# Kernel tuning notes

Hardware: AMD Instinct MI355X
Metric: run time of the kernel (lower is better)

Reference implementation:

```python
import jax, jax.numpy as jnp
import numpy as np

DIM = 512  # module's self.dim, used for the softmax scale (note: NOT head dim)

def setup_inputs() -> dict:
    key = jax.random.key(0)
    kq, kk, kv = jax.random.split(key, 3)
    shape = (4, 8, 2048, 64)  # [B, H, S, Dh]
    q = jax.random.normal(kq, shape, dtype=jnp.float32)
    k = jax.random.normal(kk, shape, dtype=jnp.float32)
    v = jax.random.normal(kv, shape, dtype=jnp.float32)
    return {"q": q, "k": k, "v": v, "n": 2048}

def reference(q, k, v, n):
    # scores = q @ k^T, then divide by sqrt(dim) AFTER matmul (as in source)
    scores = jnp.einsum('bhqd,bhkd->bhqk', q, k)
    scale = jnp.sqrt(jnp.asarray(DIM, dtype=scores.dtype))
    p_attn = jax.nn.softmax(scores / scale, axis=-1)
    return jnp.einsum('bhqk,bhkd->bhqd', p_attn, v)
```

## Files before the change

kernel.cpp:

```cpp
#include <hip/hip_runtime.h>


using half8   = __attribute__((ext_vector_type(8))) _Float16;
using half4   = __attribute__((ext_vector_type(4))) _Float16;
using half2v  = __attribute__((ext_vector_type(2))) _Float16;
using f32x4   = __attribute__((ext_vector_type(4))) float;
using f32x16  = __attribute__((ext_vector_type(16))) float;
using int4v   = __attribute__((ext_vector_type(4))) int;
using ushort8 = __attribute__((ext_vector_type(8))) unsigned short;

static __device__ __forceinline__ half2v cvt_pk(float a, float b) {
    return __builtin_bit_cast(half2v, __builtin_amdgcn_cvt_pkrtz(a, b));
}
static __device__ __forceinline__ int cvt_pk_i(float a, float b) {
    return __builtin_bit_cast(int, __builtin_amdgcn_cvt_pkrtz(a, b));
}

#define SEQ   2048
#define DH    64
#define QB    128
#define KVB   64
#define NKVT  (SEQ / KVB)
#define NITER (NKVT / 2)
#define NQB   (SEQ / QB)
#define NBH   32
#define TILE_IMG_BYTES 16384
#define QSCALE (1.4426950408889634f / 22.627416997969522f)

#if __has_builtin(__builtin_amdgcn_exp2f)
#define EXP2F __builtin_amdgcn_exp2f
#else
#define EXP2F exp2f
#endif

#define GLOAD4(dst, ptr) \
    asm volatile("global_load_dwordx4 %0, %1, off" : "=v"(dst) : "v"(ptr) : "memory")

#define WAIT_VM0()                                            \
    do {                                                      \
        asm volatile("s_waitcnt vmcnt(0)" ::: "memory");      \
        __builtin_amdgcn_sched_barrier(0);                    \
    } while (0)

#define LDS_BARRIER()                                         \
    do {                                                      \
        asm volatile("s_waitcnt lgkmcnt(0)" ::: "memory");    \
        __builtin_amdgcn_s_barrier();                         \
    } while (0)

#define LGKM_FENCE()                                          \
    do {                                                      \
        asm volatile("s_waitcnt lgkmcnt(0)" ::: "memory");    \
        __builtin_amdgcn_sched_barrier(0);                    \
    } while (0)

#define PLSWAP(a, b) \
    asm volatile("s_nop 1\n\tv_permlane32_swap_b32 %0, %1" : "+v"(a), "+v"(b))

#define MFMA32(A, B, C) __builtin_amdgcn_mfma_f32_32x32x16_f16((A), (B), (C), 0, 0, 0)

static __device__ __forceinline__ f32x16 z16() {
    f32x16 v;
#pragma unroll
    for (int i = 0; i < 16; ++i) v[i] = 0.f;
    return v;
}

#define SOFTPACK(ST0, ST1, PA)                                            \
    do {                                                                  \
        _Pragma("unroll")                                                 \
        for (int kvs2 = 0; kvs2 < 2; ++kvs2) {                            \
            const f32x16& st_ = kvs2 ? (ST1) : (ST0);                     \
            float p[16];                                                  \
            _Pragma("unroll")                                             \
            for (int r = 0; r < 16; ++r) p[r] = EXP2F(st_[r]);            \
            float s0 = 0.f, s1 = 0.f;                                     \
            _Pragma("unroll")                                             \
            for (int r = 0; r < 8; ++r) { s0 += p[r]; s1 += p[r + 8]; }   \
            lsum += s0 + s1;                                              \
            int m0 = cvt_pk_i(p[0],  p[1]),  m1 = cvt_pk_i(p[2],  p[3]);  \
            int m2 = cvt_pk_i(p[4],  p[5]),  m3 = cvt_pk_i(p[6],  p[7]);  \
            int m4 = cvt_pk_i(p[8],  p[9]),  m5 = cvt_pk_i(p[10], p[11]); \
            int m6 = cvt_pk_i(p[12], p[13]), m7 = cvt_pk_i(p[14], p[15]); \
            PLSWAP(m0, m2); PLSWAP(m1, m3);                               \
            PLSWAP(m4, m6); PLSWAP(m5, m7);                               \
            int4v t0; t0[0] = m0; t0[1] = m1; t0[2] = m2; t0[3] = m3;     \
            int4v t1; t1[0] = m4; t1[1] = m5; t1[2] = m6; t1[3] = m7;     \
            (PA)[2 * kvs2 + 0] = __builtin_bit_cast(half8, t0);           \
            (PA)[2 * kvs2 + 1] = __builtin_bit_cast(half8, t1);           \
        }                                                                 \
    } while (0)

__global__ __launch_bounds__(256)
void prep_kv(const float* __restrict__ Kg, const float* __restrict__ Vg,
             char* __restrict__ ws)
{
    __shared__ unsigned short VT[64][72];
    const int bid = blockIdx.x;
    if (bid < 4096) {
        int id   = bid * 256 + threadIdx.x;
        int col4 = id & 15;
        int row  = (id >> 4) & 63;
        int kvt  = (id >> 10) & 31;
        int bh   = id >> 15;
        f32x4 v = *(const f32x4*)(Kg + ((size_t)(bh * SEQ) + kvt * 64 + row) * DH + col4 * 4);
        half2v lo = cvt_pk(v[0], v[1]);
        half2v hi = cvt_pk(v[2], v[3]);
        half4 h; h[0] = lo[0]; h[1] = lo[1]; h[2] = hi[0]; h[3] = hi[1];
        char* out = ws + (size_t)(bh * 32 + kvt) * TILE_IMG_BYTES
                       + ((row * 128 + col4 * 8) ^ ((row & 7) << 4));
        *(half4*)out = h;
    } else {
        int tb  = bid - 4096;
        int bh  = tb >> 5;
        int kvt = tb & 31;
        int tid = threadIdx.x;

        const float* vg = Vg + (size_t)(bh * SEQ) * DH + (size_t)(kvt * 64) * DH;
#pragma unroll
        for (int rr = 0; rr < 4; ++rr) {
            int kv = rr * 16 + (tid >> 4);
            int d4 = (tid & 15) * 4;
            f32x4 v = *(const f32x4*)(vg + (size_t)kv * DH + d4);
#pragma unroll
            for (int j = 0; j < 4; ++j)
                VT[d4 + j][kv] = __builtin_bit_cast(unsigned short, (_Float16)v[j]);
        }
        __syncthreads();

        int d   = tid >> 2;
        int seg = tid & 3;
        ushort8 h0, h1;
#pragma unroll
        for (int j = 0; j < 16; ++j) {
            int off = seg * 32 + j * 2;
            int kv  = (off ^ ((d & 7) << 4)) >> 1;
            unsigned short val = VT[d][kv];
            if (j < 8) h0[j] = val; else h1[j - 8] = val;
        }
        char* out = ws + (size_t)(bh * 32 + kvt) * TILE_IMG_BYTES + 8192 + d * 128 + seg * 32;
        *(ushort8*)(out)      = h0;
        *(ushort8*)(out + 16) = h1;
    }
}

__global__ __launch_bounds__(256, 2)
void fattn_fwd(const float* __restrict__ Qg, const char* __restrict__ Wimg,
               float* __restrict__ Og)
{
    __shared__ __align__(16) char KVl[4][TILE_IMG_BYTES];

    const int tid  = threadIdx.x;
    const int lane = tid & 63;
    const int wave = tid >> 6;
    const int l31  = lane & 31;
    const int hi   = lane >> 5;

    const int wg  = blockIdx.x;
    const int swz = (wg & 7) * 64 + (wg >> 3);
    const int qb  = swz & (NQB - 1);
    const int bh  = swz >> 4;
    const size_t base = (size_t)bh * (SEQ * DH);

    half8 qfrag[4];
    {
        const int qrow = qb * QB + wave * 32 + l31;
        const float* qp = Qg + base + (size_t)qrow * DH + hi * 8;
#pragma unroll
        for (int ks = 0; ks < 4; ++ks) {
            f32x4 a = *(const f32x4*)(qp + ks * 16);
            f32x4 b = *(const f32x4*)(qp + ks * 16 + 4);
            half8 f;
#pragma unroll
            for (int i = 0; i < 4; ++i) f[i]     = (_Float16)(a[i] * QSCALE);
#pragma unroll
            for (int i = 0; i < 4; ++i) f[i + 4] = (_Float16)(b[i] * QSCALE);
            qfrag[ks] = f;
        }
    }

    f32x16 acc0 = z16(), acc1 = z16();
    float lsum = 0.f;

    const char* imgbase = Wimg + (size_t)(bh * NKVT) * TILE_IMG_BYTES;
    f32x4 kreg[8];

    auto load_pair = [&](int itp) {
        const char* img = imgbase + (size_t)(2 * itp) * TILE_IMG_BYTES;
#pragma unroll
        for (int j = 0; j < 8; ++j)
            GLOAD4(kreg[j], img + j * 4096 + tid * 16);
    };
    auto write_pair = [&](int p) {
        char* dst = KVl[2 * p];
#pragma unroll
        for (int j = 0; j < 8; ++j)
            *(f32x4*)(dst + j * 4096 + tid * 16) = kreg[j];
    };

    load_pair(0);
    WAIT_VM0();
    write_pair(0);

    for (int it = 0; it < NITER; ++it) {
        const int pair = it & 1;
        const char* kbA = KVl[2 * pair];
        const char* kbB = KVl[2 * pair + 1];

        LDS_BARRIER();

        half8 kfA[2][4], kfB[2][4];
#pragma unroll
        for (int kvs2 = 0; kvs2 < 2; ++kvs2)
#pragma unroll
            for (int ks = 0; ks < 4; ++ks) {
                int row  = kvs2 * 32 + l31;
                int byte = (row * 128 + ks * 32 + hi * 16) ^ ((row & 7) << 4);
                kfA[kvs2][ks] = *(const half8*)(kbA + byte);
                kfB[kvs2][ks] = *(const half8*)(kbB + byte);
            }
        LGKM_FENCE();

        f32x16 st0A = z16(), st1A = z16(), st0B = z16(), st1B = z16();
        __builtin_amdgcn_s_setprio(1);
#pragma unroll
        for (int ks = 0; ks < 4; ++ks) {
            st0A = MFMA32(kfA[0][ks], qfrag[ks], st0A);
            st1A = MFMA32(kfA[1][ks], qfrag[ks], st1A);
            st0B = MFMA32(kfB[0][ks], qfrag[ks], st0B);
            st1B = MFMA32(kfB[1][ks], qfrag[ks], st1B);
        }
        __builtin_amdgcn_s_setprio(0);

        half8 vfA[2][4];
#pragma unroll
        for (int ds2 = 0; ds2 < 2; ++ds2)
#pragma unroll
            for (int ks = 0; ks < 4; ++ks) {
                int row  = ds2 * 32 + l31;
                int byte = (row * 128 + ks * 32 + hi * 16) ^ ((row & 7) << 4);
                vfA[ds2][ks] = *(const half8*)(kbA + 8192 + byte);
            }
        half8 PA_A[4];
        SOFTPACK(st0A, st1A, PA_A);

        half8 vfB[2][4];
#pragma unroll
        for (int ds2 = 0; ds2 < 2; ++ds2)
#pragma unroll
            for (int ks = 0; ks < 4; ++ks) {
                int row  = ds2 * 32 + l31;
                int byte = (row * 128 + ks * 32 + hi * 16) ^ ((row & 7) << 4);
                vfB[ds2][ks] = *(const half8*)(kbB + 8192 + byte);
            }
        half8 PA_B[4];
        SOFTPACK(st0B, st1B, PA_B);

        if (it + 1 < NITER) load_pair(it + 1);

        LGKM_FENCE();

        __builtin_amdgcn_s_setprio(1);
#pragma unroll
        for (int ks = 0; ks < 4; ++ks) acc0 = MFMA32(PA_A[ks], vfA[0][ks], acc0);
#pragma unroll
        for (int ks = 0; ks < 4; ++ks) acc1 = MFMA32(PA_A[ks], vfA[1][ks], acc1);
#pragma unroll
        for (int ks = 0; ks < 4; ++ks) acc0 = MFMA32(PA_B[ks], vfB[0][ks], acc0);
#pragma unroll
        for (int ks = 0; ks < 4; ++ks) acc1 = MFMA32(PA_B[ks], vfB[1][ks], acc1);
        __builtin_amdgcn_s_setprio(0);

        if (it + 1 < NITER) {
            WAIT_VM0();
            write_pair(pair ^ 1);
        }
    }

    lsum += __shfl_xor(lsum, 32);
    const float invl = 1.f / lsum;
    const int qstrip = qb * QB + wave * 32;
#pragma unroll
    for (int r = 0; r < 16; ++r) {
        int q16 = (r & 3) + 8 * (r >> 2) + 4 * hi;
        float sc = __shfl(invl, q16);
        float* op = Og + base + (size_t)(qstrip + q16) * DH;
        op[l31]      = acc0[r] * sc;
        op[32 + l31] = acc1[r] * sc;
    }
}

extern "C" void kernel_launch(void* const* d_in, const int* in_sizes, int n_in,
                              void* d_out, int out_size, void* d_ws, size_t ws_size,
                              hipStream_t stream) {
    const float* q = (const float*)d_in[0];
    const float* k = (const float*)d_in[1];
    const float* v = (const float*)d_in[2];
    float* o = (float*)d_out;
    char* ws = (char*)d_ws;
    prep_kv<<<dim3(5120, 1, 1), dim3(256, 1, 1), 0, stream>>>(k, v, ws);
    fattn_fwd<<<dim3(NQB * NBH, 1, 1), dim3(256, 1, 1), 0, stream>>>(q, ws, o);
}
```

Before: 65.90 us.

## Process two Q strips per wave to reuse each KV tile across 256 queries

Doubles the query block to 256 rows, so each wave handles two 32-row Q strips that share the same K/V fragments loaded from LDS. The loop now walks one 64-key KV tile per iteration with a two-buffer LDS ring instead of pairs, and issues the next global load earlier. This halves the KV traffic per query and the LDS reads per MFMA. In exchange it doubles accumulator registers, drops the occupancy target to one block per CU, and halves the grid to 256 workgroups, which risks leaving CUs idle and losing latency hiding.

```diff
diff --git a/kernel.cpp b/kernel.cpp
--- a/kernel.cpp
+++ b/kernel.cpp
@@ -18,10 +18,9 @@
 
 #define SEQ   2048
 #define DH    64
-#define QB    128
+#define QB    256
 #define KVB   64
 #define NKVT  (SEQ / KVB)
-#define NITER (NKVT / 2)
 #define NQB   (SEQ / QB)
 #define NBH   32
 #define TILE_IMG_BYTES 16384
@@ -66,7 +65,7 @@
     return v;
 }
 
-#define SOFTPACK(ST0, ST1, PA)                                            \
+#define SOFTPACK(ST0, ST1, PA, LSUM)                                      \
     do {                                                                  \
         _Pragma("unroll")                                                 \
         for (int kvs2 = 0; kvs2 < 2; ++kvs2) {                            \
@@ -77,7 +76,7 @@
             float s0 = 0.f, s1 = 0.f;                                     \
             _Pragma("unroll")                                             \
             for (int r = 0; r < 8; ++r) { s0 += p[r]; s1 += p[r + 8]; }   \
-            lsum += s0 + s1;                                              \
+            (LSUM) += s0 + s1;                                            \
             int m0 = cvt_pk_i(p[0],  p[1]),  m1 = cvt_pk_i(p[2],  p[3]);  \
             int m2 = cvt_pk_i(p[4],  p[5]),  m3 = cvt_pk_i(p[6],  p[7]);  \
             int m4 = cvt_pk_i(p[8],  p[9]),  m5 = cvt_pk_i(p[10], p[11]); \
@@ -144,11 +143,11 @@
     }
 }
 
-__global__ __launch_bounds__(256, 2)
+__global__ __launch_bounds__(256, 1)
 void fattn_fwd(const float* __restrict__ Qg, const char* __restrict__ Wimg,
                float* __restrict__ Og)
 {
-    __shared__ __align__(16) char KVl[4][TILE_IMG_BYTES];
+    __shared__ __align__(16) char KVl[2][TILE_IMG_BYTES];
 
     const int tid  = threadIdx.x;
     const int lane = tid & 63;
@@ -157,14 +156,15 @@
     const int hi   = lane >> 5;
 
     const int wg  = blockIdx.x;
-    const int swz = (wg & 7) * 64 + (wg >> 3);
+    const int swz = (wg & 7) * 32 + (wg >> 3);
     const int qb  = swz & (NQB - 1);
-    const int bh  = swz >> 4;
+    const int bh  = swz >> 3;
     const size_t base = (size_t)bh * (SEQ * DH);
 
-    half8 qfrag[4];
-    {
-        const int qrow = qb * QB + wave * 32 + l31;
+    half8 qfA[4], qfB[4];
+#pragma unroll
+    for (int s = 0; s < 2; ++s) {
+        const int qrow = qb * QB + wave * 64 + s * 32 + l31;
         const float* qp = Qg + base + (size_t)qrow * DH + hi * 8;
 #pragma unroll
         for (int ks = 0; ks < 4; ++ks) {
@@ -175,118 +175,115 @@
             for (int i = 0; i < 4; ++i) f[i]     = (_Float16)(a[i] * QSCALE);
 #pragma unroll
             for (int i = 0; i < 4; ++i) f[i + 4] = (_Float16)(b[i] * QSCALE);
-            qfrag[ks] = f;
+            if (s == 0) qfA[ks] = f; else qfB[ks] = f;
         }
     }
 
-    f32x16 acc0 = z16(), acc1 = z16();
-    float lsum = 0.f;
+    f32x16 accA0 = z16(), accA1 = z16(), accB0 = z16(), accB1 = z16();
+    float lsumA = 0.f, lsumB = 0.f;
 
     const char* imgbase = Wimg + (size_t)(bh * NKVT) * TILE_IMG_BYTES;
-    f32x4 kreg[8];
-
-    auto load_pair = [&](int itp) {
-        const char* img = imgbase + (size_t)(2 * itp) * TILE_IMG_BYTES;
-#pragma unroll
-        for (int j = 0; j < 8; ++j)
+    f32x4 kreg[4];
+
+    auto load_tile = [&](int kvt) {
+        const char* img = imgbase + (size_t)kvt * TILE_IMG_BYTES;
+#pragma unroll
+        for (int j = 0; j < 4; ++j)
             GLOAD4(kreg[j], img + j * 4096 + tid * 16);
     };
-    auto write_pair = [&](int p) {
-        char* dst = KVl[2 * p];
-#pragma unroll
-        for (int j = 0; j < 8; ++j)
+    auto write_tile = [&](int b) {
+        char* dst = KVl[b];
+#pragma unroll
+        for (int j = 0; j < 4; ++j)
             *(f32x4*)(dst + j * 4096 + tid * 16) = kreg[j];
     };
 
-    load_pair(0);
+    load_tile(0);
     WAIT_VM0();
-    write_pair(0);
-
-    for (int it = 0; it < NITER; ++it) {
-        const int pair = it & 1;
-        const char* kbA = KVl[2 * pair];
-        const char* kbB = KVl[2 * pair + 1];
+    write_tile(0);
+
+    for (int kvt = 0; kvt < NKVT; ++kvt) {
+        const int cur = kvt & 1;
+        const char* kb = KVl[cur];
+        const char* vb = KVl[cur] + 8192;
+
+        if (kvt + 1 < NKVT) load_tile(kvt + 1);
 
         LDS_BARRIER();
 
-        half8 kfA[2][4], kfB[2][4];
+        half8 kf[2][4];
 #pragma unroll
         for (int kvs2 = 0; kvs2 < 2; ++kvs2)
 #pragma unroll
             for (int ks = 0; ks < 4; ++ks) {
                 int row  = kvs2 * 32 + l31;
                 int byte = (row * 128 + ks * 32 + hi * 16) ^ ((row & 7) << 4);
-                kfA[kvs2][ks] = *(const half8*)(kbA + byte);
-                kfB[kvs2][ks] = *(const half8*)(kbB + byte);
+                kf[kvs2][ks] = *(const half8*)(kb + byte);
             }
         LGKM_FENCE();
 
-        f32x16 st0A = z16(), st1A = z16(), st0B = z16(), st1B = z16();
+        f32x16 stA0 = z16(), stA1 = z16(), stB0 = z16(), stB1 = z16();
         __builtin_amdgcn_s_setprio(1);
 #pragma unroll
         for (int ks = 0; ks < 4; ++ks) {
-            st0A = MFMA32(kfA[0][ks], qfrag[ks], st0A);
-            st1A = MFMA32(kfA[1][ks], qfrag[ks], st1A);
-            st0B = MFMA32(kfB[0][ks], qfrag[ks], st0B);
-            st1B = MFMA32(kfB[1][ks], qfrag[ks], st1B);
+            stA0 = MFMA32(kf[0][ks], qfA[ks], stA0);
+            stA1 = MFMA32(kf[1][ks], qfA[ks], stA1);
+            stB0 = MFMA32(kf[0][ks], qfB[ks], stB0);
+            stB1 = MFMA32(kf[1][ks], qfB[ks], stB1);
         }
         __builtin_amdgcn_s_setprio(0);
 
-        half8 vfA[2][4];
+        half8 vf[2][4];
 #pragma unroll
         for (int ds2 = 0; ds2 < 2; ++ds2)
 #pragma unroll
             for (int ks = 0; ks < 4; ++ks) {
                 int row  = ds2 * 32 + l31;
                 int byte = (row * 128 + ks * 32 + hi * 16) ^ ((row & 7) << 4);
-                vfA[ds2][ks] = *(const half8*)(kbA + 8192 + byte);
+                vf[ds2][ks] = *(const half8*)(vb + 0 + byte);
             }
-        half8 PA_A[4];
-        SOFTPACK(st0A, st1A, PA_A);
-
-        half8 vfB[2][4];
-#pragma unroll
-        for (int ds2 = 0; ds2 < 2; ++ds2)
-#pragma unroll
-            for (int ks = 0; ks < 4; ++ks) {
-                int row  = ds2 * 32 + l31;
-                int byte = (row * 128 + ks * 32 + hi * 16) ^ ((row & 7) << 4);
-                vfB[ds2][ks] = *(const half8*)(kbB + 8192 + byte);
+
+        half8 PA_A[4], PA_B[4];
+        SOFTPACK(stA0, stA1, PA_A, lsumA);
+        SOFTPACK(stB0, stB1, PA_B, lsumB);
+
+        LGKM_FENCE();
+
+        __builtin_amdgcn_s_setprio(1);
+#pragma unroll
+        for (int ks = 0; ks < 4; ++ks) {
+            accA0 = MFMA32(PA_A[ks], vf[0][ks], accA0);
+            accA1 = MFMA32(PA_A[ks], vf[1][ks], accA1);
+            accB0 = MFMA32(PA_B[ks], vf[0][ks], accB0);
+            accB1 = MFMA32(PA_B[ks], vf[1][ks], accB1);
+        }
+        __builtin_amdgcn_s_setprio(0);
+
+        if (kvt + 1 < NKVT) {
+            WAIT_VM0();
+            write_tile(cur ^ 1);
+        }
+    }
+
+    const int qstrip = qb * QB + wave * 64;
+#pragma unroll
+    for (int s = 0; s < 2; ++s) {
+        float t = (s == 0) ? lsumA : lsumB;
+        t += __shfl_xor(t, 32);
+        float invl = 1.f / t;
+#pragma unroll
+        for (int r = 0; r < 16; ++r) {
+            int q16 = (r & 3) + 8 * (r >> 2) + 4 * hi;
+            float sc = __shfl(invl, q16);
+            float* op = Og + base + (size_t)(qstrip + s * 32 + q16) * DH;
+            if (s == 0) {
+                op[l31]      = accA0[r] * sc;
+                op[32 + l31] = accA1[r] * sc;
+            } else {
+                op[l31]      = accB0[r] * sc;
+                op[32 + l31] = accB1[r] * sc;
             }
-        half8 PA_B[4];
-        SOFTPACK(st0B, st1B, PA_B);
-
-        if (it + 1 < NITER) load_pair(it + 1);
-
-        LGKM_FENCE();
-
-        __builtin_amdgcn_s_setprio(1);
-#pragma unroll
-        for (int ks = 0; ks < 4; ++ks) acc0 = MFMA32(PA_A[ks], vfA[0][ks], acc0);
-#pragma unroll
-        for (int ks = 0; ks < 4; ++ks) acc1 = MFMA32(PA_A[ks], vfA[1][ks], acc1);
-#pragma unroll
-        for (int ks = 0; ks < 4; ++ks) acc0 = MFMA32(PA_B[ks], vfB[0][ks], acc0);
-#pragma unroll
-        for (int ks = 0; ks < 4; ++ks) acc1 = MFMA32(PA_B[ks], vfB[1][ks], acc1);
-        __builtin_amdgcn_s_setprio(0);
-
-        if (it + 1 < NITER) {
-            WAIT_VM0();
-            write_pair(pair ^ 1);
-        }
-    }
-
-    lsum += __shfl_xor(lsum, 32);
-    const float invl = 1.f / lsum;
-    const int qstrip = qb * QB + wave * 32;
-#pragma unroll
-    for (int r = 0; r < 16; ++r) {
-        int q16 = (r & 3) + 8 * (r >> 2) + 4 * hi;
-        float sc = __shfl(invl, q16);
-        float* op = Og + base + (size_t)(qstrip + q16) * DH;
-        op[l31]      = acc0[r] * sc;
-        op[32 + l31] = acc1[r] * sc;
+        }
     }
 }
 
```

Result: slower. 75.22 us (+14.2%).

## Load K/V MFMA fragments directly from global, drop LDS staging

Applied to the files above, without the earlier changes.

The prep kernel now writes K and V tiles already in per-lane MFMA fragment order, so the attention kernel can load its operands straight from global memory into registers with offset loads. The LDS buffers, barriers and LDS reads are removed. K and V loads are software-pipelined against the MFMA and softmax work using vmcnt waits. The prep kernel is merged into one block per tile that handles both K and V through LDS. The cost is that every wave re-reads K/V from L2 instead of sharing one LDS copy per workgroup, which raises global/L2 traffic fourfold.

```diff
diff --git a/kernel.cpp b/kernel.cpp
--- a/kernel.cpp
+++ b/kernel.cpp
@@ -7,7 +7,6 @@
 using f32x4   = __attribute__((ext_vector_type(4))) float;
 using f32x16  = __attribute__((ext_vector_type(16))) float;
 using int4v   = __attribute__((ext_vector_type(4))) int;
-using ushort8 = __attribute__((ext_vector_type(8))) unsigned short;
 
 static __device__ __forceinline__ half2v cvt_pk(float a, float b) {
     return __builtin_bit_cast(half2v, __builtin_amdgcn_cvt_pkrtz(a, b));
@@ -21,7 +20,6 @@
 #define QB    128
 #define KVB   64
 #define NKVT  (SEQ / KVB)
-#define NITER (NKVT / 2)
 #define NQB   (SEQ / QB)
 #define NBH   32
 #define TILE_IMG_BYTES 16384
@@ -33,25 +31,14 @@
 #define EXP2F exp2f
 #endif
 
-#define GLOAD4(dst, ptr) \
-    asm volatile("global_load_dwordx4 %0, %1, off" : "=v"(dst) : "v"(ptr) : "memory")
-
-#define WAIT_VM0()                                            \
-    do {                                                      \
-        asm volatile("s_waitcnt vmcnt(0)" ::: "memory");      \
-        __builtin_amdgcn_sched_barrier(0);                    \
-    } while (0)
-
-#define LDS_BARRIER()                                         \
-    do {                                                      \
-        asm volatile("s_waitcnt lgkmcnt(0)" ::: "memory");    \
-        __builtin_amdgcn_s_barrier();                         \
-    } while (0)
-
-#define LGKM_FENCE()                                          \
-    do {                                                      \
-        asm volatile("s_waitcnt lgkmcnt(0)" ::: "memory");    \
-        __builtin_amdgcn_sched_barrier(0);                    \
+#define GLOFF(dst, base, IMM)                                              \
+    asm volatile("global_load_dwordx4 %0, %1, off offset:" #IMM            \
+                 : "=v"(dst) : "v"(base) : "memory")
+
+#define WAIT_VM(N)                                             \
+    do {                                                       \
+        asm volatile("s_waitcnt vmcnt(" #N ")" ::: "memory");  \
+        __builtin_amdgcn_sched_barrier(0);                     \
     } while (0)
 
 #define PLSWAP(a, b) \
@@ -65,6 +52,37 @@
     for (int i = 0; i < 16; ++i) v[i] = 0.f;
     return v;
 }
+
+#define ISSUE_K(KB, kvt)                                                   \
+    do {                                                                   \
+        const char* b0_ = imgbase + (size_t)(kvt) * TILE_IMG_BYTES + lane * 16; \
+        GLOFF((KB)[0], b0_, 0);    GLOFF((KB)[1], b0_, 1024);              \
+        GLOFF((KB)[2], b0_, 2048); GLOFF((KB)[3], b0_, 3072);              \
+        const char* b1_ = b0_ + 4096;                                      \
+        GLOFF((KB)[4], b1_, 0);    GLOFF((KB)[5], b1_, 1024);              \
+        GLOFF((KB)[6], b1_, 2048); GLOFF((KB)[7], b1_, 3072);              \
+    } while (0)
+
+#define ISSUE_V(VB, kvt)                                                   \
+    do {                                                                   \
+        const char* b0_ = imgbase + (size_t)(kvt) * TILE_IMG_BYTES + 8192 + lane * 16; \
+        GLOFF((VB)[0], b0_, 0);    GLOFF((VB)[1], b0_, 1024);              \
+        GLOFF((VB)[2], b0_, 2048); GLOFF((VB)[3], b0_, 3072);              \
+        const char* b1_ = b0_ + 4096;                                      \
+        GLOFF((VB)[4], b1_, 0);    GLOFF((VB)[5], b1_, 1024);              \
+        GLOFF((VB)[6], b1_, 2048); GLOFF((VB)[7], b1_, 3072);              \
+    } while (0)
+
+#define QK_TILE(KB, ST0, ST1)                                              \
+    do {                                                                   \
+        __builtin_amdgcn_s_setprio(1);                                     \
+        _Pragma("unroll")                                                  \
+        for (int ks = 0; ks < 4; ++ks) {                                   \
+            (ST0) = MFMA32((KB)[ks],     qfrag[ks], (ST0));                \
+            (ST1) = MFMA32((KB)[4 + ks], qfrag[ks], (ST1));                \
+        }                                                                  \
+        __builtin_amdgcn_s_setprio(0);                                     \
+    } while (0)
 
 #define SOFTPACK(ST0, ST1, PA)                                            \
     do {                                                                  \
@@ -91,56 +109,56 @@
         }                                                                 \
     } while (0)
 
+#define PV_TILE(PA, VB)                                                    \
+    do {                                                                   \
+        __builtin_amdgcn_s_setprio(1);                                     \
+        _Pragma("unroll")                                                  \
+        for (int ks = 0; ks < 4; ++ks) {                                   \
+            acc0 = MFMA32((PA)[ks], (VB)[ks],     acc0);                   \
+            acc1 = MFMA32((PA)[ks], (VB)[4 + ks], acc1);                   \
+        }                                                                  \
+        __builtin_amdgcn_s_setprio(0);                                     \
+    } while (0)
+
 __global__ __launch_bounds__(256)
 void prep_kv(const float* __restrict__ Kg, const float* __restrict__ Vg,
              char* __restrict__ ws)
 {
-    __shared__ unsigned short VT[64][72];
+    __shared__ __align__(16) _Float16 Kl[64][72];
+    __shared__ __align__(16) _Float16 Vt[64][72];
+
     const int bid = blockIdx.x;
-    if (bid < 4096) {
-        int id   = bid * 256 + threadIdx.x;
-        int col4 = id & 15;
-        int row  = (id >> 4) & 63;
-        int kvt  = (id >> 10) & 31;
-        int bh   = id >> 15;
-        f32x4 v = *(const f32x4*)(Kg + ((size_t)(bh * SEQ) + kvt * 64 + row) * DH + col4 * 4);
-        half2v lo = cvt_pk(v[0], v[1]);
-        half2v hi = cvt_pk(v[2], v[3]);
-        half4 h; h[0] = lo[0]; h[1] = lo[1]; h[2] = hi[0]; h[3] = hi[1];
-        char* out = ws + (size_t)(bh * 32 + kvt) * TILE_IMG_BYTES
-                       + ((row * 128 + col4 * 8) ^ ((row & 7) << 4));
-        *(half4*)out = h;
-    } else {
-        int tb  = bid - 4096;
-        int bh  = tb >> 5;
-        int kvt = tb & 31;
-        int tid = threadIdx.x;
-
-        const float* vg = Vg + (size_t)(bh * SEQ) * DH + (size_t)(kvt * 64) * DH;
-#pragma unroll
-        for (int rr = 0; rr < 4; ++rr) {
-            int kv = rr * 16 + (tid >> 4);
-            int d4 = (tid & 15) * 4;
-            f32x4 v = *(const f32x4*)(vg + (size_t)kv * DH + d4);
-#pragma unroll
-            for (int j = 0; j < 4; ++j)
-                VT[d4 + j][kv] = __builtin_bit_cast(unsigned short, (_Float16)v[j]);
+    const int bh  = bid >> 5;
+    const int kvt = bid & 31;
+    const int tid = threadIdx.x;
+
+    const float* kg = Kg + ((size_t)bh * SEQ + (size_t)kvt * 64) * DH;
+    const float* vg = Vg + ((size_t)bh * SEQ + (size_t)kvt * 64) * DH;
+#pragma unroll
+    for (int rr = 0; rr < 4; ++rr) {
+        int row = rr * 16 + (tid >> 4);
+        int c4  = (tid & 15) * 4;
+        f32x4 kk = *(const f32x4*)(kg + (size_t)row * DH + c4);
+        f32x4 vv = *(const f32x4*)(vg + (size_t)row * DH + c4);
+#pragma unroll
+        for (int j = 0; j < 4; ++j) {
+            Kl[row][c4 + j] = (_Float16)kk[j];
+            Vt[c4 + j][row] = (_Float16)vv[j];
         }
-        __syncthreads();
-
-        int d   = tid >> 2;
-        int seg = tid & 3;
-        ushort8 h0, h1;
-#pragma unroll
-        for (int j = 0; j < 16; ++j) {
-            int off = seg * 32 + j * 2;
-            int kv  = (off ^ ((d & 7) << 4)) >> 1;
-            unsigned short val = VT[d][kv];
-            if (j < 8) h0[j] = val; else h1[j - 8] = val;
-        }
-        char* out = ws + (size_t)(bh * 32 + kvt) * TILE_IMG_BYTES + 8192 + d * 128 + seg * 32;
-        *(ushort8*)(out)      = h0;
-        *(ushort8*)(out + 16) = h1;
+    }
+    __syncthreads();
+
+    char* out = ws + (size_t)bid * TILE_IMG_BYTES;
+#pragma unroll
+    for (int rep = 0; rep < 2; ++rep) {
+        int f    = rep * 256 + tid;
+        int ln   = f & 63;
+        int ks   = (f >> 6) & 3;
+        int g2   = f >> 8;
+        int row  = g2 * 32 + (ln & 31);
+        int colh = ks * 16 + (ln >> 5) * 8;
+        *(half8*)(out + f * 16)        = *(const half8*)&Kl[row][colh];
+        *(half8*)(out + 8192 + f * 16) = *(const half8*)&Vt[row][colh];
     }
 }
 
@@ -148,8 +166,6 @@
 void fattn_fwd(const float* __restrict__ Qg, const char* __restrict__ Wimg,
                float* __restrict__ Og)
 {
-    __shared__ __align__(16) char KVl[4][TILE_IMG_BYTES];
-
     const int tid  = threadIdx.x;
     const int lane = tid & 63;
     const int wave = tid >> 6;
@@ -183,98 +199,33 @@
     float lsum = 0.f;
 
     const char* imgbase = Wimg + (size_t)(bh * NKVT) * TILE_IMG_BYTES;
-    f32x4 kreg[8];
-
-    auto load_pair = [&](int itp) {
-        const char* img = imgbase + (size_t)(2 * itp) * TILE_IMG_BYTES;
-#pragma unroll
-        for (int j = 0; j < 8; ++j)
-            GLOAD4(kreg[j], img + j * 4096 + tid * 16);
-    };
-    auto write_pair = [&](int p) {
-        char* dst = KVl[2 * p];
-#pragma unroll
-        for (int j = 0; j < 8; ++j)
-            *(f32x4*)(dst + j * 4096 + tid * 16) = kreg[j];
-    };
-
-    load_pair(0);
-    WAIT_VM0();
-    write_pair(0);
-
-    for (int it = 0; it < NITER; ++it) {
-        const int pair = it & 1;
-        const char* kbA = KVl[2 * pair];
-        const char* kbB = KVl[2 * pair + 1];
-
-        LDS_BARRIER();
-
-        half8 kfA[2][4], kfB[2][4];
-#pragma unroll
-        for (int kvs2 = 0; kvs2 < 2; ++kvs2)
-#pragma unroll
-            for (int ks = 0; ks < 4; ++ks) {
-                int row  = kvs2 * 32 + l31;
-                int byte = (row * 128 + ks * 32 + hi * 16) ^ ((row & 7) << 4);
-                kfA[kvs2][ks] = *(const half8*)(kbA + byte);
-                kfB[kvs2][ks] = *(const half8*)(kbB + byte);
-            }
-        LGKM_FENCE();
-
-        f32x16 st0A = z16(), st1A = z16(), st0B = z16(), st1B = z16();
-        __builtin_amdgcn_s_setprio(1);
-#pragma unroll
-        for (int ks = 0; ks < 4; ++ks) {
-            st0A = MFMA32(kfA[0][ks], qfrag[ks], st0A);
-            st1A = MFMA32(kfA[1][ks], qfrag[ks], st1A);
-            st0B = MFMA32(kfB[0][ks], qfrag[ks], st0B);
-            st1B = MFMA32(kfB[1][ks], qfrag[ks], st1B);
-        }
-        __builtin_amdgcn_s_setprio(0);
-
-        half8 vfA[2][4];
-#pragma unroll
-        for (int ds2 = 0; ds2 < 2; ++ds2)
-#pragma unroll
-            for (int ks = 0; ks < 4; ++ks) {
-                int row  = ds2 * 32 + l31;
-                int byte = (row * 128 + ks * 32 + hi * 16) ^ ((row & 7) << 4);
-                vfA[ds2][ks] = *(const half8*)(kbA + 8192 + byte);
-            }
-        half8 PA_A[4];
-        SOFTPACK(st0A, st1A, PA_A);
-
-        half8 vfB[2][4];
-#pragma unroll
-        for (int ds2 = 0; ds2 < 2; ++ds2)
-#pragma unroll
-            for (int ks = 0; ks < 4; ++ks) {
-                int row  = ds2 * 32 + l31;
-                int byte = (row * 128 + ks * 32 + hi * 16) ^ ((row & 7) << 4);
-                vfB[ds2][ks] = *(const half8*)(kbB + 8192 + byte);
-            }
-        half8 PA_B[4];
-        SOFTPACK(st0B, st1B, PA_B);
-
-        if (it + 1 < NITER) load_pair(it + 1);
-
-        LGKM_FENCE();
-
-        __builtin_amdgcn_s_setprio(1);
-#pragma unroll
-        for (int ks = 0; ks < 4; ++ks) acc0 = MFMA32(PA_A[ks], vfA[0][ks], acc0);
-#pragma unroll
-        for (int ks = 0; ks < 4; ++ks) acc1 = MFMA32(PA_A[ks], vfA[1][ks], acc1);
-#pragma unroll
-        for (int ks = 0; ks < 4; ++ks) acc0 = MFMA32(PA_B[ks], vfB[0][ks], acc0);
-#pragma unroll
-        for (int ks = 0; ks < 4; ++ks) acc1 = MFMA32(PA_B[ks], vfB[1][ks], acc1);
-        __builtin_amdgcn_s_setprio(0);
-
-        if (it + 1 < NITER) {
-            WAIT_VM0();
-            write_pair(pair ^ 1);
-        }
+
+    half8 kE[8], kO[8], vv[8];
+
+    ISSUE_K(kE, 0);
+    ISSUE_V(vv, 0);
+
+#pragma unroll 1
+    for (int t = 0; t < NKVT; t += 2) {
+        WAIT_VM(8);
+        f32x16 st0 = z16(), st1 = z16();
+        QK_TILE(kE, st0, st1);
+        ISSUE_K(kO, t + 1);
+        half8 PA[4];
+        SOFTPACK(st0, st1, PA);
+        WAIT_VM(8);
+        PV_TILE(PA, vv);
+        ISSUE_V(vv, t + 1);
+
+        WAIT_VM(8);
+        f32x16 su0 = z16(), su1 = z16();
+        QK_TILE(kO, su0, su1);
+        if (t + 2 < NKVT) ISSUE_K(kE, t + 2);
+        half8 PB[4];
+        SOFTPACK(su0, su1, PB);
+        if (t + 2 < NKVT) { WAIT_VM(8); } else { WAIT_VM(0); }
+        PV_TILE(PB, vv);
+        if (t + 2 < NKVT) ISSUE_V(vv, t + 2);
     }
 
     lsum += __shfl_xor(lsum, 32);
@@ -298,6 +249,6 @@
     const float* v = (const float*)d_in[2];
     float* o = (float*)d_out;
     char* ws = (char*)d_ws;
-    prep_kv<<<dim3(5120, 1, 1), dim3(256, 1, 1), 0, stream>>>(k, v, ws);
+    prep_kv<<<dim3(NBH * NKVT, 1, 1), dim3(256, 1, 1), 0, stream>>>(k, v, ws);
     fattn_fwd<<<dim3(NQB * NBH, 1, 1), dim3(256, 1, 1), 0, stream>>>(q, ws, o);
 }
```

Measured after the change: 63.83 us. -3.1%, faster.
